# Optimization experiments

Measured on AMD Instinct MI355X. Metric: run time of the kernel, lower is better.

Reference implementation:

```python
import jax, jax.numpy as jnp
import numpy as np

PADDING_VALUE = 0.0  # padding_value init arg


def setup_inputs() -> dict:
    key = jax.random.key(0)
    k1, k2 = jax.random.split(key)
    B, T, D = 16, 4096, 256
    x = jax.random.normal(k1, (B, T, D), dtype=jnp.float32)
    mask = jax.random.bernoulli(k2, 0.5, (B, T))  # bool
    return {"x": x, "mask": mask}


def reference(x, mask):
    # batch_first=True: x is [B, T, ...feat], mask is [B, T].
    B, T = mask.shape
    lens = mask.sum(axis=1)  # [B] number of selected elements per row
    # Stable argsort on (~mask) brings indices of True entries to the front,
    # preserving their original order -> index of the j-th True element.
    order = jnp.argsort(jnp.logical_not(mask), axis=1, stable=True)  # [B, T]
    # Gather x rows into compacted order.
    idx = order.reshape(order.shape + (1,) * (x.ndim - 2))  # [B, T, 1...]
    gathered = jnp.take_along_axis(x, idx, axis=1)  # [B, T, ...feat]
    # Right-pad positions j >= lens[b] with padding_value.
    valid = jnp.arange(T)[None, :] < lens[:, None]  # [B, T]
    valid = valid.reshape(valid.shape + (1,) * (x.ndim - 2))
    x_ = jnp.where(valid, gathered, jnp.asarray(PADDING_VALUE, x.dtype))
    return x_, lens
```

## Files before the change

kernel.cpp:

```cpp
#include <hip/hip_runtime.h>


typedef float f32x4 __attribute__((ext_vector_type(4)));

#define BLK 256
#define NW (BLK / 64)
#define ROWS 64

__global__ __launch_bounds__(BLK) void pad_masked_fused(
    const float* __restrict__ x,
    const int* __restrict__ mask,
    float* __restrict__ out,
    float* __restrict__ lens_f,
    int T, int D4) {

    const int b = blockIdx.x;
    const int c = blockIdx.y;
    const int tid = threadIdx.x;
    const int lane = tid & 63;
    const int wave = tid >> 6;
    const int j0 = c * ROWS;

    const int* mrow = mask + (size_t)b * T;

    int pre = 0, all = 0;
    for (int e = tid * 4; e < T; e += BLK * 4) {
        const int4 mv = *reinterpret_cast<const int4*>(mrow + e);
        const int s4 = (mv.x != 0) + (mv.y != 0) + (mv.z != 0) + (mv.w != 0);
        all += s4;
        if (e < j0) pre += s4;
    }
    unsigned long long packed = (unsigned long long)(unsigned)pre |
                                ((unsigned long long)(unsigned)all << 32);
    #pragma unroll
    for (int off = 32; off; off >>= 1) packed += __shfl_xor(packed, off);

    __shared__ unsigned long long wred[NW];
    __shared__ int selRows[ROWS];
    __shared__ int nsel;
    if (lane == 0) wred[wave] = packed;
    __syncthreads();

    unsigned long long tot = 0;
    #pragma unroll
    for (int w = 0; w < NW; ++w) tot += wred[w];
    const int P = (int)(tot & 0xffffffffull);
    const int L = (int)(tot >> 32);

    if (wave == 0) {
        const int m = (mrow[j0 + lane] != 0);
        int incl = m;
        #pragma unroll
        for (int off = 1; off < 64; off <<= 1) {
            const int v = __shfl_up(incl, off);
            if (lane >= off) incl += v;
        }
        if (m) selRows[incl - 1] = lane;
        if (lane == 63) nsel = incl;
    }
    __syncthreads();
    const int n = nsel;

    if (c == 0 && tid == 0) lens_f[b] = (float)L;

    const f32x4* xrow = reinterpret_cast<const f32x4*>(x) +
                        ((size_t)b * T + j0) * (size_t)D4;
    f32x4* obase = reinterpret_cast<f32x4*>(out) + (size_t)b * T * (size_t)D4;
    const f32x4 z = {0.f, 0.f, 0.f, 0.f};

    for (int i = wave; i < n; i += 2 * NW) {
        const int i2 = i + NW;
        const bool h2 = (i2 < n);
        const int r0 = selRows[i];
        const int r1 = h2 ? selRows[i2] : 0;
        for (int t = lane; t < D4; t += 64) {
            const f32x4 v0 = xrow[(size_t)r0 * D4 + t];
            f32x4 v1 = z;
            if (h2) v1 = xrow[(size_t)r1 * D4 + t];
            obase[(size_t)(P + i) * D4 + t] = v0;
            if (h2) obase[(size_t)(P + i2) * D4 + t] = v1;
        }
    }

    const int zstart = (L > j0) ? L : j0;
    for (int j = zstart + wave; j < j0 + ROWS; j += NW) {
        for (int t = lane; t < D4; t += 64)
            obase[(size_t)j * D4 + t] = z;
    }
}

extern "C" void kernel_launch(void* const* d_in, const int* in_sizes, int n_in,
                              void* d_out, int out_size, void* d_ws, size_t ws_size,
                              hipStream_t stream) {
    const float* x = (const float*)d_in[0];
    const int* mask = (const int*)d_in[1];

    const int Nx = in_sizes[0];
    const int BT = in_sizes[1];
    const int B = out_size - Nx;
    const int T = BT / B;
    const int D = Nx / BT;
    const int D4 = D / 4;

    float* out = (float*)d_out;
    float* lens_f = out + (size_t)Nx;

    dim3 grid(B, T / ROWS);
    pad_masked_fused<<<grid, BLK, 0, stream>>>(x, mask, out, lens_f, T, D4);
}
```

Before: 21.11 us.

## Add specialized pipelined kernel that prefetches selected rows before mask reduction

Adds a templated kernel for D=256, used at these test sizes, that uses a ballot bitmask in place of a shared-memory scan to find selected rows. Each wave issues up to twelve row loads into registers before the mask prefix-count reduction and barrier, so gather latency overlaps the reduction. Mask loads are fully unrolled by a compile-time iteration count. The cost is higher register pressure, bounded by launch bounds with a minimum of four blocks, and the general kernel is kept as a fallback.

Measured after the change: 19.66 us. -6.9%, faster.

```diff
diff --git a/kernel.cpp b/kernel.cpp
--- a/kernel.cpp
+++ b/kernel.cpp
@@ -6,6 +6,97 @@
 #define BLK 256
 #define NW (BLK / 64)
 #define ROWS 64
+#define PF 12
+
+template <int NITER>
+__global__ __launch_bounds__(BLK, 4) void pad_masked_pipe(
+    const float* __restrict__ x,
+    const int* __restrict__ mask,
+    float* __restrict__ out,
+    float* __restrict__ lens_f,
+    int T, int D4) {
+
+    const int b = blockIdx.x;
+    const int c = blockIdx.y;
+    const int tid = threadIdx.x;
+    const int lane = tid & 63;
+    const int wave = tid >> 6;
+    const int j0 = c * ROWS;
+
+    const int* mrow = mask + (size_t)b * T;
+
+    const int msel = (mrow[j0 + lane] != 0);
+
+    int4 mv[NITER];
+    #pragma unroll
+    for (int k = 0; k < NITER; ++k)
+        mv[k] = *reinterpret_cast<const int4*>(mrow + (size_t)(tid + k * BLK) * 4);
+
+    const unsigned long long sel = __ballot(msel);
+    const f32x4* xrow = reinterpret_cast<const f32x4*>(x) +
+                        ((size_t)b * T + j0) * (size_t)D4;
+
+    unsigned long long t = sel;
+    #pragma unroll
+    for (int k = 0; k < NW - 1; ++k)
+        if (k < wave) t &= t - 1;
+
+    f32x4 v[PF];
+    int cnt = 0;
+    #pragma unroll
+    for (int k = 0; k < PF; ++k) {
+        if (t) {
+            const int r = (int)__builtin_ctzll(t);
+            v[k] = xrow[(size_t)r * 64 + lane];
+            cnt = k + 1;
+            #pragma unroll
+            for (int p = 0; p < NW; ++p) t &= t - 1;
+        }
+    }
+
+    int pre = 0, all = 0;
+    #pragma unroll
+    for (int k = 0; k < NITER; ++k) {
+        const int4 m4 = mv[k];
+        const int s4 = (m4.x != 0) + (m4.y != 0) + (m4.z != 0) + (m4.w != 0);
+        all += s4;
+        if ((tid + k * BLK) * 4 < j0) pre += s4;
+    }
+    unsigned long long packed = (unsigned long long)(unsigned)pre |
+                                ((unsigned long long)(unsigned)all << 32);
+    #pragma unroll
+    for (int off = 32; off; off >>= 1) packed += __shfl_xor(packed, off);
+
+    __shared__ unsigned long long wred[NW];
+    if (lane == 0) wred[wave] = packed;
+    __syncthreads();
+    unsigned long long tot = 0;
+    #pragma unroll
+    for (int w = 0; w < NW; ++w) tot += wred[w];
+    const int P = (int)(tot & 0xffffffffull);
+    const int L = (int)(tot >> 32);
+
+    if (c == 0 && tid == 0) lens_f[b] = (float)L;
+
+    f32x4* obase = reinterpret_cast<f32x4*>(out) + (size_t)b * T * (size_t)D4;
+    #pragma unroll
+    for (int k = 0; k < PF; ++k)
+        if (k < cnt)
+            obase[(size_t)(P + wave + k * NW) * 64 + lane] = v[k];
+    int i = wave + PF * NW;
+    while (t) {
+        const int r = (int)__builtin_ctzll(t);
+        #pragma unroll
+        for (int p = 0; p < NW; ++p) t &= t - 1;
+        obase[(size_t)(P + i) * 64 + lane] = xrow[(size_t)r * 64 + lane];
+        i += NW;
+    }
+
+    const f32x4 z = {0.f, 0.f, 0.f, 0.f};
+    const int zstart = (L > j0) ? L : j0;
+    for (int j = zstart + wave; j < j0 + ROWS; j += NW)
+        obase[(size_t)j * 64 + lane] = z;
+}
 
 __global__ __launch_bounds__(BLK) void pad_masked_fused(
     const float* __restrict__ x,
@@ -40,7 +131,6 @@
     __shared__ int nsel;
     if (lane == 0) wred[wave] = packed;
     __syncthreads();
-
     unsigned long long tot = 0;
     #pragma unroll
     for (int w = 0; w < NW; ++w) tot += wred[w];
@@ -73,20 +163,19 @@
         const bool h2 = (i2 < n);
         const int r0 = selRows[i];
         const int r1 = h2 ? selRows[i2] : 0;
-        for (int t = lane; t < D4; t += 64) {
-            const f32x4 v0 = xrow[(size_t)r0 * D4 + t];
+        for (int tt = lane; tt < D4; tt += 64) {
+            const f32x4 v0 = xrow[(size_t)r0 * D4 + tt];
             f32x4 v1 = z;
-            if (h2) v1 = xrow[(size_t)r1 * D4 + t];
-            obase[(size_t)(P + i) * D4 + t] = v0;
-            if (h2) obase[(size_t)(P + i2) * D4 + t] = v1;
+            if (h2) v1 = xrow[(size_t)r1 * D4 + tt];
+            obase[(size_t)(P + i) * D4 + tt] = v0;
+            if (h2) obase[(size_t)(P + i2) * D4 + tt] = v1;
         }
     }
 
     const int zstart = (L > j0) ? L : j0;
-    for (int j = zstart + wave; j < j0 + ROWS; j += NW) {
-        for (int t = lane; t < D4; t += 64)
-            obase[(size_t)j * D4 + t] = z;
-    }
+    for (int j = zstart + wave; j < j0 + ROWS; j += NW)
+        for (int tt = lane; tt < D4; tt += 64)
+            obase[(size_t)j * D4 + tt] = z;
 }
 
 extern "C" void kernel_launch(void* const* d_in, const int* in_sizes, int n_in,
@@ -106,5 +195,17 @@
     float* lens_f = out + (size_t)Nx;
 
     dim3 grid(B, T / ROWS);
-    pad_masked_fused<<<grid, BLK, 0, stream>>>(x, mask, out, lens_f, T, D4);
+
+    const int niter = T / (BLK * 4);
+    const bool fast = (D4 == 64) && (T % (BLK * 4) == 0) && (T % ROWS == 0);
+    if (fast && niter == 4)
+        pad_masked_pipe<4><<<grid, BLK, 0, stream>>>(x, mask, out, lens_f, T, D4);
+    else if (fast && niter == 2)
+        pad_masked_pipe<2><<<grid, BLK, 0, stream>>>(x, mask, out, lens_f, T, D4);
+    else if (fast && niter == 1)
+        pad_masked_pipe<1><<<grid, BLK, 0, stream>>>(x, mask, out, lens_f, T, D4);
+    else if (fast && niter == 8)
+        pad_masked_pipe<8><<<grid, BLK, 0, stream>>>(x, mask, out, lens_f, T, D4);
+    else
+        pad_masked_fused<<<grid, BLK, 0, stream>>>(x, mask, out, lens_f, T, D4);
 }
```
